# Optimization experiments

Measured on AMD Instinct MI355X. Metric: run time of the kernel, lower is better.

The kernel has to match this reference:

```python
import jax, jax.numpy as jnp
import numpy as np

C = 1.0          # curvature
TOP_K = 5
LAMBDA_H = 0.01
TAU = 0.1        # forward default
NEG_SAMPLES = 20 # forward default
EPS = 1e-9
B, D = 4096, 64


def _to_ball(v):
    # map gaussian vectors strictly inside the unit Poincare ball
    return 0.8 * v / (1.0 + jnp.linalg.norm(v, axis=-1, keepdims=True))


def setup_inputs() -> dict:
    key = jax.random.key(0)
    ka, kt = jax.random.split(key)
    audio = _to_ball(jax.random.normal(ka, (B, D), dtype=jnp.float32))
    text = _to_ball(jax.random.normal(kt, (B, D), dtype=jnp.float32))
    return {"audio_embeds": audio, "text_embeds": text}


def _pairwise_poincare(x, y, c=C):
    # ||x-y||^2 via gemm instead of materializing [N,N,D] diff tensor
    x_sq = jnp.sum(x * x, axis=-1, keepdims=True)          # [N,1]
    y_sq = jnp.sum(y * y, axis=-1, keepdims=True).T        # [1,M]
    diff_sq = jnp.maximum(x_sq + y_sq - 2.0 * (x @ y.T), 0.0)
    x_cl = jnp.minimum(x_sq, 1.0 - EPS)
    y_cl = jnp.minimum(y_sq, 1.0 - EPS)
    denom = jnp.maximum((1.0 - x_cl) * (1.0 - y_cl), EPS)
    z = jnp.maximum(1.0 + 2.0 * diff_sq / denom, 1.0 + EPS)
    return jnp.arccosh(z) / jnp.sqrt(jnp.asarray(c, x.dtype))


def _topk_triplet(embeds, key):
    n = embeds.shape[0]
    dist = _pairwise_poincare(embeds, embeds)
    dist = dist.at[jnp.arange(n), jnp.arange(n)].set(jnp.inf)  # fill_diagonal_(inf)
    k = min(TOP_K, n - 1)
    neg_pos, pos_idx = jax.lax.top_k(-dist, k)                 # k smallest distances
    pos_term = jax.scipy.special.logsumexp(neg_pos / TAU, axis=1)  # logsumexp(-pos_dist/tau)
    # mask out top-k positives (diagonal stays in pool, holding +inf -> exp(-inf)=0)
    mask = jnp.ones((n, n), bool).at[jnp.arange(n)[:, None], pos_idx].set(False)
    # stable argsort: mask-True columns first, in original column order -> matches dist[i][mask[i]]
    order = jnp.argsort(jnp.where(mask, 0, 1), axis=1)
    pool = jnp.take_along_axis(dist, order[:, : n - k], axis=1)    # [n, n-k]
    samp = jax.random.randint(key, (n, NEG_SAMPLES), 0, n - k)
    neg_vals = jnp.take_along_axis(pool, samp, axis=1)             # [n, NEG_SAMPLES]
    neg_term = jax.scipy.special.logsumexp(-neg_vals / TAU, axis=1)
    return jnp.mean(neg_term - pos_term)  # mean of -(pos_term - neg_term)


def reference(audio_embeds, text_embeds):
    # HyperbolicLayeredLoss.forward returns lambda_h * (text_h + audio_h);
    # the cross-modal loss is computed but NOT added to the returned total in the source.
    key_text = jax.random.key(1)
    key_audio = jax.random.key(2)
    loss_text_h = _topk_triplet(text_embeds, key_text)
    loss_audio_h = _topk_triplet(audio_embeds, key_audio)
    return LAMBDA_H * (loss_text_h + loss_audio_h)
```

## Files before the change

### kernel.cpp

```cpp
#include <hip/hip_runtime.h>
#include <stdint.h>

#define JAX_PARTITIONABLE 1

constexpr int N = 4096;
constexpr int DIM = 64;
constexpr int TOPK = 5;
constexpr int NEGS = 20;
constexpr float TAU_ = 0.1f;
constexpr uint32_t SPAN = 4091u;
constexpr uint32_t MULT = 2309u;

constexpr int CQ = 256;
constexpr int NSLAB = N / CQ;
constexpr int NT = CQ / 16;
constexpr int RPB = 64;
constexpr int YSTRIDE = 136;
constexpr int CAP = 32;

typedef __attribute__((ext_vector_type(8))) short bf16x8;
typedef __attribute__((ext_vector_type(4))) float f32x4;

__device__ __forceinline__ uint32_t rotl32(uint32_t v, int d) {
  return (v << d) | (v >> (32 - d));
}

__device__ __forceinline__ void threefry(uint32_t k0, uint32_t k1,
                                         uint32_t& x0, uint32_t& x1) {
  const uint32_t k2 = k0 ^ k1 ^ 0x1BD11BDAu;
  x0 += k0; x1 += k1;
#define TF_R(r) { x0 += x1; x1 = rotl32(x1, r); x1 ^= x0; }
  TF_R(13) TF_R(15) TF_R(26) TF_R(6)
  x0 += k1; x1 += k2 + 1u;
  TF_R(17) TF_R(29) TF_R(16) TF_R(24)
  x0 += k2; x1 += k0 + 2u;
  TF_R(13) TF_R(15) TF_R(26) TF_R(6)
  x0 += k0; x1 += k1 + 3u;
  TF_R(17) TF_R(29) TF_R(16) TF_R(24)
  x0 += k1; x1 += k2 + 4u;
  TF_R(13) TF_R(15) TF_R(26) TF_R(6)
  x0 += k2; x1 += k0 + 5u;
#undef TF_R
}

__device__ __forceinline__ uint32_t sample_idx(uint32_t seed, uint32_t f) {
#if JAX_PARTITIONABLE
  uint32_t a0 = 0u, a1 = 0u; threefry(0u, seed, a0, a1);
  uint32_t b0 = 0u, b1 = 1u; threefry(0u, seed, b0, b1);
  uint32_t h0 = 0u, h1 = f;  threefry(a0, a1, h0, h1);
  const uint32_t hi = h0 ^ h1;
  uint32_t l0 = 0u, l1 = f;  threefry(b0, b1, l0, l1);
  const uint32_t lo = l0 ^ l1;
#else
  uint32_t a0 = 0u, a1 = 2u; threefry(0u, seed, a0, a1);
  uint32_t c0 = 1u, c1 = 3u; threefry(0u, seed, c0, c1);
  const uint32_t HALF = (uint32_t)(N * NEGS / 2);
  uint32_t hi, lo;
  if (f < HALF) {
    uint32_t x0 = f, x1 = f + HALF; threefry(a0, c0, x0, x1); hi = x0;
    x0 = f; x1 = f + HALF;          threefry(a1, c1, x0, x1); lo = x0;
  } else {
    uint32_t x0 = f - HALF, x1 = f; threefry(a0, c0, x0, x1); hi = x1;
    x0 = f - HALF; x1 = f;          threefry(a1, c1, x0, x1); lo = x1;
  }
#endif
  return ((hi % SPAN) * MULT + (lo % SPAN)) % SPAN;
}

__device__ __forceinline__ float acosh_dev(float z) {
  return logf(z + sqrtf((z - 1.0f) * (z + 1.0f)));
}

__device__ __forceinline__ uint16_t f2bf(float f) {
  const uint32_t u = __float_as_uint(f);
  return (uint16_t)((u + 0x7FFFu + ((u >> 16) & 1u)) >> 16);
}
__device__ __forceinline__ float bf2f(uint16_t h) {
  return __uint_as_float((uint32_t)h << 16);
}

__global__ __launch_bounds__(64) void k_pre(const float* __restrict__ Xa,
                                            const float* __restrict__ Xt,
                                            uint16_t* __restrict__ Xs,
                                            float* __restrict__ ysq,
                                            float* __restrict__ inv,
                                            uint32_t* __restrict__ cnt) {
  const int m = blockIdx.y;
  const float* __restrict__ X = (m == 0) ? Xt : Xa;
  const int i = blockIdx.x * 64 + threadIdx.x;
  const float* xr = X + (size_t)i * DIM;

  uint32_t hb[DIM / 2], lb[DIM / 2];
  float s = 0.0f;
#pragma unroll
  for (int u = 0; u < DIM / 4; ++u) {
    const float4 v = *(const float4*)(xr + 4 * u);
    s = fmaf(v.x, v.x, s); s = fmaf(v.y, v.y, s);
    s = fmaf(v.z, v.z, s); s = fmaf(v.w, v.w, s);
    const uint16_t h0 = f2bf(v.x), h1 = f2bf(v.y), h2 = f2bf(v.z), h3 = f2bf(v.w);
    const uint16_t l0 = f2bf(v.x - bf2f(h0)), l1 = f2bf(v.y - bf2f(h1));
    const uint16_t l2 = f2bf(v.z - bf2f(h2)), l3 = f2bf(v.w - bf2f(h3));
    hb[2 * u]     = (uint32_t)h0 | ((uint32_t)h1 << 16);
    hb[2 * u + 1] = (uint32_t)h2 | ((uint32_t)h3 << 16);
    lb[2 * u]     = (uint32_t)l0 | ((uint32_t)l1 << 16);
    lb[2 * u + 1] = (uint32_t)l2 | ((uint32_t)l3 << 16);
  }
  uint32_t* dst = (uint32_t*)(Xs + (size_t)(m * N + i) * 128);
#pragma unroll
  for (int w = 0; w < 8; ++w) {
    uint4 qh = { hb[4 * w], hb[4 * w + 1], hb[4 * w + 2], hb[4 * w + 3] };
    ((uint4*)dst)[w] = qh;
  }
#pragma unroll
  for (int w = 0; w < 8; ++w) {
    uint4 ql = { lb[4 * w], lb[4 * w + 1], lb[4 * w + 2], lb[4 * w + 3] };
    ((uint4*)dst)[8 + w] = ql;
  }
  ysq[m * N + i] = s;
  inv[m * N + i] = 1.0f / (1.0f - fminf(s, 1.0f));
  cnt[m * N + i] = 0u;
}

__global__ __launch_bounds__(256) void k_zb(
    const uint16_t* __restrict__ Xs, const float* __restrict__ ysq,
    const float* __restrict__ inv, float* __restrict__ zb5) {
  const int rb = (int)blockIdx.x;
  const int qq = (int)blockIdx.y;
  const int m = (int)blockIdx.z;
  const int j0q = qq * CQ;

  const int tid = (int)threadIdx.x;
  const int wid = tid >> 6;
  const int l = tid & 63;
  const int i0w = rb * RPB + wid * 16;
  const int mN = m * N;
  const uint16_t* __restrict__ Xm = Xs + (size_t)m * N * 128;
  const int lc = l & 15;
  const int lk = l >> 4;
  const int lk4 = lk * 4;
  const int lk8 = lk * 8;
  const int sr = tid >> 4;
  const int sc8 = (tid & 15) * 8;
  const int gi = i0w + lc;

  __shared__ __align__(16) unsigned char smem[4 * 16 * YSTRIDE * 2 + 2048];
  uint16_t* ybuf = (uint16_t*)smem;
  float* sq_s = (float*)(smem + 4 * 16 * YSTRIDE * 2);
  float* iv_s = sq_s + CQ;

  bf16x8 xf[2][2];
#pragma unroll
  for (int c = 0; c < 2; ++c)
#pragma unroll
    for (int h = 0; h < 2; ++h)
      xf[c][h] = *(const bf16x8*)(Xm + (size_t)gi * 128 + h * 64 + c * 32 + lk8);

  const float xsq_i = ysq[mN + gi];
  const float inv2_i = 2.0f * inv[mN + gi];

  float t5f[TOPK];
#pragma unroll
  for (int t = 0; t < TOPK; ++t) t5f[t] = __uint_as_float(0x7F800000u);

  const f32x4 zz = {0.0f, 0.0f, 0.0f, 0.0f};
  const float INF_ = __uint_as_float(0x7F800000u);

  {
    if (tid < 64)
      *(float4*)&sq_s[tid * 4] = *(const float4*)&ysq[mN + j0q + tid * 4];
    else if (tid < 128)
      *(float4*)&iv_s[(tid - 64) * 4] =
          *(const float4*)&inv[mN + j0q + (tid - 64) * 4];
    *(uint4*)(ybuf + sr * YSTRIDE + sc8) =
        *(const uint4*)(Xm + (size_t)(j0q + sr) * 128 + sc8);
    *(uint4*)(ybuf + 16 * YSTRIDE + sr * YSTRIDE + sc8) =
        *(const uint4*)(Xm + (size_t)(j0q + 16 + sr) * 128 + sc8);
    __syncthreads();
  }

#define PZB(T, BUF)                                                            \
  {                                                                            \
    const uint16_t* yp = (BUF) + lc * YSTRIDE + lk8;                           \
    const bf16x8 Y0 = *(const bf16x8*)(yp);                                    \
    const bf16x8 Y1 = *(const bf16x8*)(yp + 32);                               \
    const bf16x8 Y2 = *(const bf16x8*)(yp + 64);                               \
    const bf16x8 Y3 = *(const bf16x8*)(yp + 96);                               \
    f32x4 acc;               \
    acc = __builtin_amdgcn_mfma_f32_16x16x32_bf16(Y0, xf[0][0], zz, 0, 0, 0);  \
    acc = __builtin_amdgcn_mfma_f32_16x16x32_bf16(Y1, xf[1][0], acc, 0, 0, 0); \
    acc = __builtin_amdgcn_mfma_f32_16x16x32_bf16(Y2, xf[0][0], acc, 0, 0, 0); \
    acc = __builtin_amdgcn_mfma_f32_16x16x32_bf16(Y3, xf[1][0], acc, 0, 0, 0); \
    acc = __builtin_amdgcn_mfma_f32_16x16x32_bf16(Y0, xf[0][1], acc, 0, 0, 0); \
    acc = __builtin_amdgcn_mfma_f32_16x16x32_bf16(Y1, xf[1][1], acc, 0, 0, 0); \
    const float4 sq4 = *(const float4*)&sq_s[(T) * 16 + lk4];                  \
    const float4 iv4 = *(const float4*)&iv_s[(T) * 16 + lk4];                  \
    const int jb = j0q + (T) * 16;                                             \
    float zt[4];                                                               \
    _Pragma("unroll") for (int p = 0; p < 4; ++p) {                            \
      const float yc = (p == 0) ? sq4.x : (p == 1) ? sq4.y                     \
                      : (p == 2) ? sq4.z : sq4.w;                              \
      const float ic = (p == 0) ? iv4.x : (p == 1) ? iv4.y                     \
                      : (p == 2) ? iv4.z : iv4.w;                              \
      const float diff = fmaxf(xsq_i + yc - 2.0f * acc[p], 0.0f);              \
      zt[p] = fmaf(diff * inv2_i, ic, 1.0f);                                   \
    }                                                                          \
    if (jb == i0w) {                           \
      _Pragma("unroll") for (int p = 0; p < 4; ++p)                            \
        if (gi == jb + lk4 + p) zt[p] = INF_;                                  \
    }                                                                          \
    _Pragma("unroll") for (int p = 0; p < 4; ++p) {                            \
      float v = zt[p];              \
      _Pragma("unroll") for (int t = 0; t < TOPK; ++t) {                       \
        const float mn = fminf(t5f[t], v);                                     \
        v = fmaxf(t5f[t], v);                                                  \
        t5f[t] = mn;                                                           \
      }                                                                        \
    }                                                                          \
  }

#pragma unroll 1
  for (int T = 0; T < NT; T += 2) {
    const bool hn = (T + 2 < NT);
    uint4 s2, s3;
    if (hn) {
      s2 = *(const uint4*)(Xm + (size_t)(j0q + (T + 2) * 16 + sr) * 128 + sc8);
      s3 = *(const uint4*)(Xm + (size_t)(j0q + (T + 3) * 16 + sr) * 128 + sc8);
    }
    PZB(T, ybuf + (size_t)((T) & 3) * 16 * YSTRIDE)
    PZB(T + 1, ybuf + (size_t)((T + 1) & 3) * 16 * YSTRIDE)
    if (hn) {
      *(uint4*)(ybuf + (size_t)((T + 2) & 3) * 16 * YSTRIDE + sr * YSTRIDE + sc8) = s2;
      *(uint4*)(ybuf + (size_t)((T + 3) & 3) * 16 * YSTRIDE + sr * YSTRIDE + sc8) = s3;
    }
    __syncthreads();
  }
#undef PZB

  float* mb = (float*)smem;
#pragma unroll
  for (int t = 0; t < TOPK; ++t)
    mb[((size_t)(wid * 16) + lc) * 21 + lk * TOPK + t] = t5f[t];
  __syncthreads();

  if (l < 16) {
    float cur[TOPK];
#pragma unroll
    for (int t = 0; t < TOPK; ++t) cur[t] = mb[((size_t)(wid * 16) + l) * 21 + t];
    for (int c = 1; c < 4; ++c) {
      for (int t = 0; t < TOPK; ++t) {
        float v = mb[((size_t)(wid * 16) + l) * 21 + c * TOPK + t];
        if (v >= cur[TOPK - 1]) break;
#pragma unroll
        for (int u = 0; u < TOPK; ++u) {
          const float mn = fminf(cur[u], v);
          v = fmaxf(cur[u], v);
          cur[u] = mn;
        }
      }
    }
#pragma unroll
    for (int t = 0; t < TOPK; ++t)
      zb5[((size_t)(m * NSLAB + qq) * N + i0w + l) * TOPK + t] = cur[t];
  }
}

__global__ __launch_bounds__(256) void k_zmerge(const float* __restrict__ zb5,
                                                float* __restrict__ bound) {
  const int r = (int)blockIdx.x * 256 + (int)threadIdx.x;
  const int m = r >> 12;
  const int row = r & (N - 1);
  float cur[TOPK];
#pragma unroll
  for (int t = 0; t < TOPK; ++t)
    cur[t] = zb5[((size_t)(m * NSLAB) * N + row) * TOPK + t];
  for (int s = 1; s < NSLAB; ++s) {
    for (int t = 0; t < TOPK; ++t) {
      float v = zb5[((size_t)(m * NSLAB + s) * N + row) * TOPK + t];
      if (v >= cur[TOPK - 1]) break;
#pragma unroll
      for (int u = 0; u < TOPK; ++u) {
        const float mn = fminf(cur[u], v);
        v = fmaxf(cur[u], v);
        cur[u] = mn;
      }
    }
  }
  bound[r] = cur[TOPK - 1];
}

__global__ __launch_bounds__(256) void k_scan(
    const uint16_t* __restrict__ Xs, const float* __restrict__ ysq,
    const float* __restrict__ inv, const float* __restrict__ bound,
    uint32_t* __restrict__ cnt, uint64_t* __restrict__ rowlist) {
  const int rb = (int)blockIdx.x;
  const int qq = (int)blockIdx.y;
  const int m = (int)blockIdx.z;
  const int j0q = qq * CQ;

  const int tid = (int)threadIdx.x;
  const int wid = tid >> 6;
  const int l = tid & 63;
  const int i0w = rb * RPB + wid * 16;
  const int mN = m * N;
  const uint16_t* __restrict__ Xm = Xs + (size_t)m * N * 128;
  const int lc = l & 15;
  const int lk = l >> 4;
  const int lk4 = lk * 4;
  const int lk8 = lk * 8;
  const int sr = tid >> 4;
  const int sc8 = (tid & 15) * 8;
  const int gi = i0w + lc;

  __shared__ __align__(16) unsigned char smem[4 * 16 * YSTRIDE * 2 + 2048];
  uint16_t* ybuf = (uint16_t*)smem;
  float* sq_s = (float*)(smem + 4 * 16 * YSTRIDE * 2);
  float* iv_s = sq_s + CQ;

  bf16x8 xf[2][2];
#pragma unroll
  for (int c = 0; c < 2; ++c)
#pragma unroll
    for (int h = 0; h < 2; ++h)
      xf[c][h] = *(const bf16x8*)(Xm + (size_t)gi * 128 + h * 64 + c * 32 + lk8);

  const float xsq_i = ysq[mN + gi];
  const float inv2_i = 2.0f * inv[mN + gi];
  const float bz = bound[mN + gi];

  const f32x4 zz = {0.0f, 0.0f, 0.0f, 0.0f};
  const float INF_ = __uint_as_float(0x7F800000u);

  {
    if (tid < 64)
      *(float4*)&sq_s[tid * 4] = *(const float4*)&ysq[mN + j0q + tid * 4];
    else if (tid < 128)
      *(float4*)&iv_s[(tid - 64) * 4] =
          *(const float4*)&inv[mN + j0q + (tid - 64) * 4];
    *(uint4*)(ybuf + sr * YSTRIDE + sc8) =
        *(const uint4*)(Xm + (size_t)(j0q + sr) * 128 + sc8);
    *(uint4*)(ybuf + 16 * YSTRIDE + sr * YSTRIDE + sc8) =
        *(const uint4*)(Xm + (size_t)(j0q + 16 + sr) * 128 + sc8);
    __syncthreads();
  }

#define PSCAN(T, BUF)                                                          \
  {                                                                            \
    const uint16_t* yp = (BUF) + lc * YSTRIDE + lk8;                           \
    const bf16x8 Y0 = *(const bf16x8*)(yp);                                    \
    const bf16x8 Y1 = *(const bf16x8*)(yp + 32);                               \
    const bf16x8 Y2 = *(const bf16x8*)(yp + 64);                               \
    const bf16x8 Y3 = *(const bf16x8*)(yp + 96);                               \
    f32x4 acc;                        \
    acc = __builtin_amdgcn_mfma_f32_16x16x32_bf16(Y0, xf[0][0], zz, 0, 0, 0);  \
    acc = __builtin_amdgcn_mfma_f32_16x16x32_bf16(Y1, xf[1][0], acc, 0, 0, 0); \
    acc = __builtin_amdgcn_mfma_f32_16x16x32_bf16(Y2, xf[0][0], acc, 0, 0, 0); \
    acc = __builtin_amdgcn_mfma_f32_16x16x32_bf16(Y3, xf[1][0], acc, 0, 0, 0); \
    acc = __builtin_amdgcn_mfma_f32_16x16x32_bf16(Y0, xf[0][1], acc, 0, 0, 0); \
    acc = __builtin_amdgcn_mfma_f32_16x16x32_bf16(Y1, xf[1][1], acc, 0, 0, 0); \
    const float4 sq4 = *(const float4*)&sq_s[(T) * 16 + lk4];                  \
    const float4 iv4 = *(const float4*)&iv_s[(T) * 16 + lk4];                  \
    const int jb = j0q + (T) * 16;                                             \
    float zt[4];                                                               \
    _Pragma("unroll") for (int p = 0; p < 4; ++p) {                            \
      const float yc = (p == 0) ? sq4.x : (p == 1) ? sq4.y                     \
                      : (p == 2) ? sq4.z : sq4.w;                              \
      const float ic = (p == 0) ? iv4.x : (p == 1) ? iv4.y                     \
                      : (p == 2) ? iv4.z : iv4.w;                              \
      const float diff = fmaxf(xsq_i + yc - 2.0f * acc[p], 0.0f);              \
      zt[p] = fmaf(diff * inv2_i, ic, 1.0f);                                   \
    }                                                                          \
    if (jb == i0w) {                           \
      _Pragma("unroll") for (int p = 0; p < 4; ++p)                            \
        if (gi == jb + lk4 + p) zt[p] = INF_;                                  \
    }                                                                          \
    const float zm = fminf(fminf(zt[0], zt[1]), fminf(zt[2], zt[3]));          \
    if (zm <= bz) {                                                            \
      _Pragma("unroll") for (int p = 0; p < 4; ++p) {                          \
        if (zt[p] <= bz) {                                                     \
          const uint64_t key = ((uint64_t)__float_as_uint(zt[p]) << 32) |      \
                               (uint32_t)(jb + lk4 + p);                       \
          const uint32_t slot = atomicAdd(&cnt[mN + gi], 1u);                  \
          if (slot < (uint32_t)CAP)                                            \
            rowlist[(size_t)(mN + gi) * CAP + slot] = key;                     \
        }                                                                      \
      }                                                                        \
    }                                                                          \
  }

#pragma unroll 1
  for (int T = 0; T < NT; T += 2) {
    const bool hn = (T + 2 < NT);
    uint4 s2, s3;
    if (hn) {
      s2 = *(const uint4*)(Xm + (size_t)(j0q + (T + 2) * 16 + sr) * 128 + sc8);
      s3 = *(const uint4*)(Xm + (size_t)(j0q + (T + 3) * 16 + sr) * 128 + sc8);
    }
    PSCAN(T, ybuf + (size_t)((T) & 3) * 16 * YSTRIDE)
    PSCAN(T + 1, ybuf + (size_t)((T + 1) & 3) * 16 * YSTRIDE)
    if (hn) {
      *(uint4*)(ybuf + (size_t)((T + 2) & 3) * 16 * YSTRIDE + sr * YSTRIDE + sc8) = s2;
      *(uint4*)(ybuf + (size_t)((T + 3) & 3) * 16 * YSTRIDE + sr * YSTRIDE + sc8) = s3;
    }
    __syncthreads();
  }
#undef PSCAN
}

__global__ __launch_bounds__(64) void k_neg(const float* __restrict__ Xa,
                                            const float* __restrict__ Xt,
                                            const float* __restrict__ ysq,
                                            const float* __restrict__ inv,
                                            const uint32_t* __restrict__ cnt,
                                            const uint64_t* __restrict__ rowlist,
                                            float* __restrict__ rowres) {
  const int m = blockIdx.y;
  const int i = blockIdx.x;
  const float* __restrict__ X = (m == 0) ? Xt : Xa;
  const uint32_t seed = (m == 0) ? 1u : 2u;
  const int lane = threadIdx.x;

  __shared__ float4 xi4[DIM / 4];
  __shared__ float posv[TOPK];
  if (lane < DIM / 4) xi4[lane] = ((const float4*)(X + (size_t)i * DIM))[lane];
  __syncthreads();

  const uint64_t SENT = ((uint64_t)0x7F800000u << 32) | 0xFFFFFFFFu;
  uint64_t cur[TOPK];
#pragma unroll
  for (int t = 0; t < TOPK; ++t) cur[t] = SENT;
  {
    const uint32_t c_ = min(cnt[m * N + i], (uint32_t)CAP);
    for (uint32_t sv = 0; sv < c_; ++sv) {
      uint64_t key = rowlist[(size_t)(m * N + i) * CAP + sv];
      if (key < cur[TOPK - 1]) {
#pragma unroll
        for (int u = 0; u < TOPK; ++u) {
          const uint64_t cv = cur[u];
          if (key < cv) { cur[u] = key; key = cv; }
        }
      }
    }
  }

  const float ysq_i = ysq[m * N + i];
  const float inv_i = inv[m * N + i];

  if (lane >= 32 && lane < 32 + TOPK) {
    const int t = lane - 32;
    const uint32_t c = (uint32_t)(cur[t] & 0xffffffffu);
    const float4* xc = (const float4*)(X + (size_t)c * DIM);
    float dot = 0.0f;
#pragma unroll
    for (int k = 0; k < DIM / 4; ++k) {
      const float4 a = xi4[k];
      const float4 b = xc[k];
      dot = fmaf(a.x, b.x, dot); dot = fmaf(a.y, b.y, dot);
      dot = fmaf(a.z, b.z, dot); dot = fmaf(a.w, b.w, dot);
    }
    const float diff = fmaxf(ysq_i + ysq[m * N + c] - 2.0f * dot, 0.0f);
    const float z = 1.0f + 2.0f * diff * inv_i * inv[m * N + c];
    posv[t] = -acosh_dev(z) / TAU_;
  }

  uint32_t pidx[TOPK];
#pragma unroll
  for (int t = 0; t < TOPK; ++t) pidx[t] = (uint32_t)(cur[t] & 0xffffffffu);

#define CSWAP(a, b)                                                           \
  { const uint32_t mn = pidx[a] < pidx[b] ? pidx[a] : pidx[b];                \
    const uint32_t mx = pidx[a] < pidx[b] ? pidx[b] : pidx[a];                \
    pidx[a] = mn; pidx[b] = mx; }
  CSWAP(0, 1) CSWAP(3, 4) CSWAP(2, 4) CSWAP(2, 3) CSWAP(1, 4)
  CSWAP(0, 3) CSWAP(0, 2) CSWAP(1, 3) CSWAP(1, 2)
#undef CSWAP

  float v = -1e30f;
  if (lane < NEGS) {
    const uint32_t f = (uint32_t)i * (uint32_t)NEGS + (uint32_t)lane;
    uint32_t c = sample_idx(seed, f);
#pragma unroll
    for (int t = 0; t < TOPK; ++t) c += (c >= pidx[t]) ? 1u : 0u;
    if (c != (uint32_t)i) {
      const float4* xc = (const float4*)(X + (size_t)c * DIM);
      float dot = 0.0f;
#pragma unroll
      for (int k = 0; k < DIM / 4; ++k) {
        const float4 a = xi4[k];
        const float4 b = xc[k];
        dot = fmaf(a.x, b.x, dot); dot = fmaf(a.y, b.y, dot);
        dot = fmaf(a.z, b.z, dot); dot = fmaf(a.w, b.w, dot);
      }
      const float diff = fmaxf(ysq_i + ysq[m * N + c] - 2.0f * dot, 0.0f);
      const float z = 1.0f + 2.0f * diff * inv_i * inv[m * N + c];
      v = -acosh_dev(z) / TAU_;
    }
  }

  __syncthreads();

  float vmax = v;
#pragma unroll
  for (int o = 32; o > 0; o >>= 1) vmax = fmaxf(vmax, __shfl_xor(vmax, o, 64));
  float e = expf(v - vmax);
  float ss = e;
#pragma unroll
  for (int o = 32; o > 0; o >>= 1) ss += __shfl_xor(ss, o, 64);

  if (lane == 0) {
    float vm = -1e30f;
#pragma unroll
    for (int t = 0; t < TOPK; ++t) vm = fmaxf(vm, posv[t]);
    float ps = 0.0f;
#pragma unroll
    for (int t = 0; t < TOPK; ++t) ps += expf(posv[t] - vm);
    const float pos = vm + logf(ps);
    rowres[m * N + i] = (vmax + logf(ss)) - pos;
  }
}

__global__ __launch_bounds__(256) void k_reduce(const float* __restrict__ rowres,
                                                float* __restrict__ out) {
  __shared__ double sh[256];
  double s = 0.0;
  for (int idx = threadIdx.x; idx < 2 * N; idx += 256) s += (double)rowres[idx];
  sh[threadIdx.x] = s;
  __syncthreads();
  for (int o = 128; o > 0; o >>= 1) {
    if (threadIdx.x < o) sh[threadIdx.x] += sh[threadIdx.x + o];
    __syncthreads();
  }
  if (threadIdx.x == 0) out[0] = (float)(0.01 * (sh[0] / (double)N));
}

extern "C" void kernel_launch(void* const* d_in, const int* in_sizes, int n_in,
                              void* d_out, int out_size, void* d_ws,
                              size_t ws_size, hipStream_t stream) {
  const float* Xa = (const float*)d_in[0];
  const float* Xt = (const float*)d_in[1];
  float* out = (float*)d_out;

  float* ysq = (float*)d_ws;
  float* inv = ysq + 2 * N;
  float* bound = inv + 2 * N;
  float* rowres = bound + 2 * N;
  uint32_t* cnt = (uint32_t*)(rowres + 2 * N);
  float* zb5 = (float*)(cnt + 2 * N);
  uint64_t* rowlist = (uint64_t*)(zb5 + (size_t)2 * NSLAB * N * TOPK);
  uint16_t* Xs = (uint16_t*)(rowlist + (size_t)2 * N * CAP);

  k_pre<<<dim3(N / 64, 2), 64, 0, stream>>>(Xa, Xt, Xs, ysq, inv, cnt);
  k_zb<<<dim3(N / RPB, NSLAB, 2), 256, 0, stream>>>(Xs, ysq, inv, zb5);
  k_zmerge<<<(2 * N) / 256, 256, 0, stream>>>(zb5, bound);
  k_scan<<<dim3(N / RPB, NSLAB, 2), 256, 0, stream>>>(Xs, ysq, inv, bound, cnt,
                                                      rowlist);
  k_neg<<<dim3(N, 2), 64, 0, stream>>>(Xa, Xt, ysq, inv, cnt, rowlist, rowres);
  k_reduce<<<1, 256, 0, stream>>>(rowres, out);
}
```

Measured before the change: 103.5 us.

## Sample four column slabs for top-k bound, fuse merge into scan, precompute RNG keys

The bound-estimation pass now covers only 4 of the 16 column slabs, which gives a looser per-row top-5 threshold. The separate merge kernel is removed and each scan block merges the 4 partial results for its rows in shared memory. The scan compares a monotone surrogate (clamped squared distance times the column's inverse factor) instead of the full z value. The candidate list capacity grows to absorb the extra survivors a looser bound lets through. Threefry key derivation moves to compile-time constants, and the risk is list overflow if more than 256 candidates pass the bound.

```diff
diff --git a/kernel.cpp b/kernel.cpp
--- a/kernel.cpp
+++ b/kernel.cpp
@@ -1,7 +1,5 @@
 #include <hip/hip_runtime.h>
 #include <stdint.h>
-
-#define JAX_PARTITIONABLE 1
 
 constexpr int N = 4096;
 constexpr int DIM = 64;
@@ -16,15 +14,39 @@
 constexpr int NT = CQ / 16;
 constexpr int RPB = 64;
 constexpr int YSTRIDE = 136;
-constexpr int CAP = 32;
+constexpr int NSAMP = 4;
+constexpr int CAP = 256;
 
 typedef __attribute__((ext_vector_type(8))) short bf16x8;
 typedef __attribute__((ext_vector_type(4))) float f32x4;
 
+struct U2 { uint32_t a, b; };
+
+constexpr U2 tf20(uint32_t k0, uint32_t k1, uint32_t x0, uint32_t x1) {
+  const uint32_t k2 = k0 ^ k1 ^ 0x1BD11BDAu;
+  x0 += k0; x1 += k1;
+#define TF_C(r) { x0 += x1; x1 = (x1 << (r)) | (x1 >> (32 - (r))); x1 ^= x0; }
+  TF_C(13) TF_C(15) TF_C(26) TF_C(6)
+  x0 += k1; x1 += k2 + 1u;
+  TF_C(17) TF_C(29) TF_C(16) TF_C(24)
+  x0 += k2; x1 += k0 + 2u;
+  TF_C(13) TF_C(15) TF_C(26) TF_C(6)
+  x0 += k0; x1 += k1 + 3u;
+  TF_C(17) TF_C(29) TF_C(16) TF_C(24)
+  x0 += k1; x1 += k2 + 4u;
+  TF_C(13) TF_C(15) TF_C(26) TF_C(6)
+  x0 += k2; x1 += k0 + 5u;
+#undef TF_C
+  return {x0, x1};
+}
+constexpr U2 KT1 = tf20(0u, 1u, 0u, 0u);
+constexpr U2 KT2 = tf20(0u, 1u, 0u, 1u);
+constexpr U2 KA1 = tf20(0u, 2u, 0u, 0u);
+constexpr U2 KA2 = tf20(0u, 2u, 0u, 1u);
+
 __device__ __forceinline__ uint32_t rotl32(uint32_t v, int d) {
   return (v << d) | (v >> (32 - d));
 }
-
 __device__ __forceinline__ void threefry(uint32_t k0, uint32_t k1,
                                          uint32_t& x0, uint32_t& x1) {
   const uint32_t k2 = k0 ^ k1 ^ 0x1BD11BDAu;
@@ -43,34 +65,17 @@
 #undef TF_R
 }
 
-__device__ __forceinline__ uint32_t sample_idx(uint32_t seed, uint32_t f) {
-#if JAX_PARTITIONABLE
-  uint32_t a0 = 0u, a1 = 0u; threefry(0u, seed, a0, a1);
-  uint32_t b0 = 0u, b1 = 1u; threefry(0u, seed, b0, b1);
-  uint32_t h0 = 0u, h1 = f;  threefry(a0, a1, h0, h1);
+__device__ __forceinline__ uint32_t sample_idx(U2 K1, U2 K2, uint32_t f) {
+  uint32_t h0 = 0u, h1 = f; threefry(K1.a, K1.b, h0, h1);
   const uint32_t hi = h0 ^ h1;
-  uint32_t l0 = 0u, l1 = f;  threefry(b0, b1, l0, l1);
+  uint32_t l0 = 0u, l1 = f; threefry(K2.a, K2.b, l0, l1);
   const uint32_t lo = l0 ^ l1;
-#else
-  uint32_t a0 = 0u, a1 = 2u; threefry(0u, seed, a0, a1);
-  uint32_t c0 = 1u, c1 = 3u; threefry(0u, seed, c0, c1);
-  const uint32_t HALF = (uint32_t)(N * NEGS / 2);
-  uint32_t hi, lo;
-  if (f < HALF) {
-    uint32_t x0 = f, x1 = f + HALF; threefry(a0, c0, x0, x1); hi = x0;
-    x0 = f; x1 = f + HALF;          threefry(a1, c1, x0, x1); lo = x0;
-  } else {
-    uint32_t x0 = f - HALF, x1 = f; threefry(a0, c0, x0, x1); hi = x1;
-    x0 = f - HALF; x1 = f;          threefry(a1, c1, x0, x1); lo = x1;
-  }
-#endif
   return ((hi % SPAN) * MULT + (lo % SPAN)) % SPAN;
 }
 
 __device__ __forceinline__ float acosh_dev(float z) {
   return logf(z + sqrtf((z - 1.0f) * (z + 1.0f)));
 }
-
 __device__ __forceinline__ uint16_t f2bf(float f) {
   const uint32_t u = __float_as_uint(f);
   return (uint16_t)((u + 0x7FFFu + ((u >> 16) & 1u)) >> 16);
@@ -121,13 +126,13 @@
   cnt[m * N + i] = 0u;
 }
 
-__global__ __launch_bounds__(256) void k_zb(
+__global__ __launch_bounds__(256) void k_zb4(
     const uint16_t* __restrict__ Xs, const float* __restrict__ ysq,
     const float* __restrict__ inv, float* __restrict__ zb5) {
   const int rb = (int)blockIdx.x;
-  const int qq = (int)blockIdx.y;
+  const int qs = (int)blockIdx.y;
   const int m = (int)blockIdx.z;
-  const int j0q = qq * CQ;
+  const int j0q = (qs * 4 + 1) * CQ;
 
   const int tid = (int)threadIdx.x;
   const int wid = tid >> 6;
@@ -157,6 +162,7 @@
 
   const float xsq_i = ysq[mN + gi];
   const float inv2_i = 2.0f * inv[mN + gi];
+  (void)inv2_i;
 
   float t5f[TOPK];
 #pragma unroll
@@ -185,7 +191,7 @@
     const bf16x8 Y1 = *(const bf16x8*)(yp + 32);                               \
     const bf16x8 Y2 = *(const bf16x8*)(yp + 64);                               \
     const bf16x8 Y3 = *(const bf16x8*)(yp + 96);                               \
-    f32x4 acc;               \
+    f32x4 acc;        \
     acc = __builtin_amdgcn_mfma_f32_16x16x32_bf16(Y0, xf[0][0], zz, 0, 0, 0);  \
     acc = __builtin_amdgcn_mfma_f32_16x16x32_bf16(Y1, xf[1][0], acc, 0, 0, 0); \
     acc = __builtin_amdgcn_mfma_f32_16x16x32_bf16(Y2, xf[0][0], acc, 0, 0, 0); \
@@ -195,21 +201,21 @@
     const float4 sq4 = *(const float4*)&sq_s[(T) * 16 + lk4];                  \
     const float4 iv4 = *(const float4*)&iv_s[(T) * 16 + lk4];                  \
     const int jb = j0q + (T) * 16;                                             \
-    float zt[4];                                                               \
+    float st[4];                                                               \
     _Pragma("unroll") for (int p = 0; p < 4; ++p) {                            \
       const float yc = (p == 0) ? sq4.x : (p == 1) ? sq4.y                     \
                       : (p == 2) ? sq4.z : sq4.w;                              \
       const float ic = (p == 0) ? iv4.x : (p == 1) ? iv4.y                     \
                       : (p == 2) ? iv4.z : iv4.w;                              \
-      const float diff = fmaxf(xsq_i + yc - 2.0f * acc[p], 0.0f);              \
-      zt[p] = fmaf(diff * inv2_i, ic, 1.0f);                                   \
+      const float d = fmaf(-2.0f, acc[p], xsq_i + yc);                         \
+      st[p] = fmaxf(d, 0.0f) * ic;         \
     }                                                                          \
     if (jb == i0w) {                           \
       _Pragma("unroll") for (int p = 0; p < 4; ++p)                            \
-        if (gi == jb + lk4 + p) zt[p] = INF_;                                  \
+        if (gi == jb + lk4 + p) st[p] = INF_;                                  \
     }                                                                          \
     _Pragma("unroll") for (int p = 0; p < 4; ++p) {                            \
-      float v = zt[p];              \
+      float v = st[p];              \
       _Pragma("unroll") for (int t = 0; t < TOPK; ++t) {                       \
         const float mn = fminf(t5f[t], v);                                     \
         v = fmaxf(t5f[t], v);                                                  \
@@ -260,37 +266,13 @@
     }
 #pragma unroll
     for (int t = 0; t < TOPK; ++t)
-      zb5[((size_t)(m * NSLAB + qq) * N + i0w + l) * TOPK + t] = cur[t];
-  }
-}
-
-__global__ __launch_bounds__(256) void k_zmerge(const float* __restrict__ zb5,
-                                                float* __restrict__ bound) {
-  const int r = (int)blockIdx.x * 256 + (int)threadIdx.x;
-  const int m = r >> 12;
-  const int row = r & (N - 1);
-  float cur[TOPK];
-#pragma unroll
-  for (int t = 0; t < TOPK; ++t)
-    cur[t] = zb5[((size_t)(m * NSLAB) * N + row) * TOPK + t];
-  for (int s = 1; s < NSLAB; ++s) {
-    for (int t = 0; t < TOPK; ++t) {
-      float v = zb5[((size_t)(m * NSLAB + s) * N + row) * TOPK + t];
-      if (v >= cur[TOPK - 1]) break;
-#pragma unroll
-      for (int u = 0; u < TOPK; ++u) {
-        const float mn = fminf(cur[u], v);
-        v = fmaxf(cur[u], v);
-        cur[u] = mn;
-      }
-    }
-  }
-  bound[r] = cur[TOPK - 1];
+      zb5[((size_t)(m * NSAMP + qs) * N + i0w + l) * TOPK + t] = cur[t];
+  }
 }
 
 __global__ __launch_bounds__(256) void k_scan(
     const uint16_t* __restrict__ Xs, const float* __restrict__ ysq,
-    const float* __restrict__ inv, const float* __restrict__ bound,
+    const float* __restrict__ inv, const float* __restrict__ zb5,
     uint32_t* __restrict__ cnt, uint64_t* __restrict__ rowlist) {
   const int rb = (int)blockIdx.x;
   const int qq = (int)blockIdx.y;
@@ -300,7 +282,8 @@
   const int tid = (int)threadIdx.x;
   const int wid = tid >> 6;
   const int l = tid & 63;
-  const int i0w = rb * RPB + wid * 16;
+  const int i0b = rb * RPB;
+  const int i0w = i0b + wid * 16;
   const int mN = m * N;
   const uint16_t* __restrict__ Xm = Xs + (size_t)m * N * 128;
   const int lc = l & 15;
@@ -312,6 +295,7 @@
   const int gi = i0w + lc;
 
   __shared__ __align__(16) unsigned char smem[4 * 16 * YSTRIDE * 2 + 2048];
+  __shared__ float bs_s[RPB];
   uint16_t* ybuf = (uint16_t*)smem;
   float* sq_s = (float*)(smem + 4 * 16 * YSTRIDE * 2);
   float* iv_s = sq_s + CQ;
@@ -324,24 +308,43 @@
       xf[c][h] = *(const bf16x8*)(Xm + (size_t)gi * 128 + h * 64 + c * 32 + lk8);
 
   const float xsq_i = ysq[mN + gi];
-  const float inv2_i = 2.0f * inv[mN + gi];
-  const float bz = bound[mN + gi];
 
   const f32x4 zz = {0.0f, 0.0f, 0.0f, 0.0f};
   const float INF_ = __uint_as_float(0x7F800000u);
 
   {
-    if (tid < 64)
+    if (tid < 64) {
+      const int row = i0b + tid;
+      float cur[TOPK];
+#pragma unroll
+      for (int t = 0; t < TOPK; ++t)
+        cur[t] = zb5[((size_t)(m * NSAMP) * N + row) * TOPK + t];
+      for (int q = 1; q < NSAMP; ++q) {
+        for (int t = 0; t < TOPK; ++t) {
+          float v = zb5[((size_t)(m * NSAMP + q) * N + row) * TOPK + t];
+          if (v >= cur[TOPK - 1]) break;
+#pragma unroll
+          for (int u = 0; u < TOPK; ++u) {
+            const float mn = fminf(cur[u], v);
+            v = fmaxf(cur[u], v);
+            cur[u] = mn;
+          }
+        }
+      }
+      bs_s[tid] = cur[TOPK - 1];
       *(float4*)&sq_s[tid * 4] = *(const float4*)&ysq[mN + j0q + tid * 4];
-    else if (tid < 128)
+    } else if (tid < 128) {
       *(float4*)&iv_s[(tid - 64) * 4] =
           *(const float4*)&inv[mN + j0q + (tid - 64) * 4];
+    }
     *(uint4*)(ybuf + sr * YSTRIDE + sc8) =
         *(const uint4*)(Xm + (size_t)(j0q + sr) * 128 + sc8);
     *(uint4*)(ybuf + 16 * YSTRIDE + sr * YSTRIDE + sc8) =
         *(const uint4*)(Xm + (size_t)(j0q + 16 + sr) * 128 + sc8);
     __syncthreads();
   }
+
+  const float bz = bs_s[wid * 16 + lc];
 
 #define PSCAN(T, BUF)                                                          \
   {                                                                            \
@@ -360,24 +363,24 @@
     const float4 sq4 = *(const float4*)&sq_s[(T) * 16 + lk4];                  \
     const float4 iv4 = *(const float4*)&iv_s[(T) * 16 + lk4];                  \
     const int jb = j0q + (T) * 16;                                             \
-    float zt[4];                                                               \
+    float st[4];                                                               \
     _Pragma("unroll") for (int p = 0; p < 4; ++p) {                            \
       const float yc = (p == 0) ? sq4.x : (p == 1) ? sq4.y                     \
                       : (p == 2) ? sq4.z : sq4.w;                              \
       const float ic = (p == 0) ? iv4.x : (p == 1) ? iv4.y                     \
                       : (p == 2) ? iv4.z : iv4.w;                              \
-      const float diff = fmaxf(xsq_i + yc - 2.0f * acc[p], 0.0f);              \
-      zt[p] = fmaf(diff * inv2_i, ic, 1.0f);                                   \
+      const float d = fmaf(-2.0f, acc[p], xsq_i + yc);                         \
+      st[p] = fmaxf(d, 0.0f) * ic;                                             \
     }                                                                          \
     if (jb == i0w) {                           \
       _Pragma("unroll") for (int p = 0; p < 4; ++p)                            \
-        if (gi == jb + lk4 + p) zt[p] = INF_;                                  \
+        if (gi == jb + lk4 + p) st[p] = INF_;                                  \
     }                                                                          \
-    const float zm = fminf(fminf(zt[0], zt[1]), fminf(zt[2], zt[3]));          \
-    if (zm <= bz) {                                                            \
+    const float sm = fminf(fminf(st[0], st[1]), fminf(st[2], st[3]));          \
+    if (sm <= bz) {                                                            \
       _Pragma("unroll") for (int p = 0; p < 4; ++p) {                          \
-        if (zt[p] <= bz) {                                                     \
-          const uint64_t key = ((uint64_t)__float_as_uint(zt[p]) << 32) |      \
+        if (st[p] <= bz) {                                                     \
+          const uint64_t key = ((uint64_t)__float_as_uint(st[p]) << 32) |      \
                                (uint32_t)(jb + lk4 + p);                       \
           const uint32_t slot = atomicAdd(&cnt[mN + gi], 1u);                  \
           if (slot < (uint32_t)CAP)                                            \
@@ -416,7 +419,8 @@
   const int m = blockIdx.y;
   const int i = blockIdx.x;
   const float* __restrict__ X = (m == 0) ? Xt : Xa;
-  const uint32_t seed = (m == 0) ? 1u : 2u;
+  const U2 K1 = (m == 0) ? KT1 : KA1;
+  const U2 K2 = (m == 0) ? KT2 : KA2;
   const int lane = threadIdx.x;
 
   __shared__ float4 xi4[DIM / 4];
@@ -477,7 +481,7 @@
   float v = -1e30f;
   if (lane < NEGS) {
     const uint32_t f = (uint32_t)i * (uint32_t)NEGS + (uint32_t)lane;
-    uint32_t c = sample_idx(seed, f);
+    uint32_t c = sample_idx(K1, K2, f);
 #pragma unroll
     for (int t = 0; t < TOPK; ++t) c += (c >= pidx[t]) ? 1u : 0u;
     if (c != (uint32_t)i) {
@@ -541,17 +545,15 @@
 
   float* ysq = (float*)d_ws;
   float* inv = ysq + 2 * N;
-  float* bound = inv + 2 * N;
-  float* rowres = bound + 2 * N;
+  float* rowres = inv + 2 * N;
   uint32_t* cnt = (uint32_t*)(rowres + 2 * N);
   float* zb5 = (float*)(cnt + 2 * N);
-  uint64_t* rowlist = (uint64_t*)(zb5 + (size_t)2 * NSLAB * N * TOPK);
+  uint64_t* rowlist = (uint64_t*)(zb5 + (size_t)2 * NSAMP * N * TOPK);
   uint16_t* Xs = (uint16_t*)(rowlist + (size_t)2 * N * CAP);
 
   k_pre<<<dim3(N / 64, 2), 64, 0, stream>>>(Xa, Xt, Xs, ysq, inv, cnt);
-  k_zb<<<dim3(N / RPB, NSLAB, 2), 256, 0, stream>>>(Xs, ysq, inv, zb5);
-  k_zmerge<<<(2 * N) / 256, 256, 0, stream>>>(zb5, bound);
-  k_scan<<<dim3(N / RPB, NSLAB, 2), 256, 0, stream>>>(Xs, ysq, inv, bound, cnt,
+  k_zb4<<<dim3(N / RPB, NSAMP, 2), 256, 0, stream>>>(Xs, ysq, inv, zb5);
+  k_scan<<<dim3(N / RPB, NSLAB, 2), 256, 0, stream>>>(Xs, ysq, inv, zb5, cnt,
                                                       rowlist);
   k_neg<<<dim3(N, 2), 64, 0, stream>>>(Xa, Xt, ysq, inv, cnt, rowlist, rowres);
   k_reduce<<<1, 256, 0, stream>>>(rowres, out);
```

After: 101.4 us. 2.1% less time.
